# Optimization experiments

Measured on AMD Instinct MI355X. Metric: run time of the kernel, lower is better.

Reference implementation:

```python
import jax, jax.numpy as jnp
import numpy as np

D_MODEL = 1024
NUM_HEADS = 16
D_K = D_MODEL // NUM_HEADS


def setup_inputs() -> dict:
    key = jax.random.key(0)
    ks = jax.random.split(key, 5)
    scale = 1.0 / np.sqrt(D_MODEL)
    x = jax.random.normal(ks[0], (4, 2048, D_MODEL), dtype=jnp.float32)
    W_qkv = jax.random.normal(ks[1], (D_MODEL, 3 * D_MODEL), dtype=jnp.float32) * scale
    b_qkv = jax.random.normal(ks[2], (3 * D_MODEL,), dtype=jnp.float32) * 0.02
    W_o = jax.random.normal(ks[3], (D_MODEL, D_MODEL), dtype=jnp.float32) * scale
    b_o = jax.random.normal(ks[4], (D_MODEL,), dtype=jnp.float32) * 0.02
    return {"x": x, "W_qkv": W_qkv, "b_qkv": b_qkv, "W_o": W_o, "b_o": b_o}


def reference(x, W_qkv, b_qkv, W_o, b_o):
    B, S, _ = x.shape
    qkv = x @ W_qkv + b_qkv  # [B, S, 3*D]
    q, k, v = jnp.split(qkv, 3, axis=-1)
    # [B, H, S, d_k]
    q = q.reshape(B, S, NUM_HEADS, D_K).transpose(0, 2, 1, 3)
    k = k.reshape(B, S, NUM_HEADS, D_K).transpose(0, 2, 1, 3)
    v = v.reshape(B, S, NUM_HEADS, D_K).transpose(0, 2, 1, 3)
    scores = jnp.einsum("bhqd,bhkd->bhqk", q, k) / jnp.sqrt(jnp.float32(D_K))
    causal = jnp.tril(jnp.ones((S, S), dtype=bool))  # [S, S]
    scores = jnp.where(causal[None, None], scores, jnp.float32(-1e9))
    attn = jax.nn.softmax(scores, axis=-1)
    out = jnp.einsum("bhqk,bhkd->bhqd", attn, v)  # [B, H, S, d_k]
    out = out.transpose(0, 2, 1, 3).reshape(B, S, D_MODEL)
    return out @ W_o + b_o
```

## Files before the change

kernel.cpp:

```cpp
#include <hip/hip_runtime.h>
#include <cstdint>
#include <cstddef>

typedef __bf16 bf16x8 __attribute__((ext_vector_type(8)));
typedef __bf16 bf16x4 __attribute__((ext_vector_type(4)));
typedef short s16x4 __attribute__((ext_vector_type(4)));
typedef float f32x4 __attribute__((ext_vector_type(4)));

__device__ __forceinline__ ushort f2bf(float f) {
  union { float f; uint32_t u; } v; v.f = f;
  uint32_t r = (v.u + 0x7fffu + ((v.u >> 16) & 1u)) >> 16;
  return (ushort)r;
}

__device__ __forceinline__ float fast_exp2(float x) {
#if defined(__HIP_DEVICE_COMPILE__) && __has_builtin(__builtin_amdgcn_exp2f)
  return __builtin_amdgcn_exp2f(x);
#else
  return exp2f(x);
#endif
}

__device__ __forceinline__ f32x4 mfma16(bf16x4 a, bf16x4 b, f32x4 c) {
#if defined(__HIP_DEVICE_COMPILE__)
#if __has_builtin(__builtin_amdgcn_mfma_f32_16x16x16_bf16)
  return __builtin_amdgcn_mfma_f32_16x16x16_bf16(a, b, c, 0, 0, 0);
#else
  return __builtin_amdgcn_mfma_f32_16x16x16bf16_1k(
      __builtin_bit_cast(s16x4, a), __builtin_bit_cast(s16x4, b), c, 0, 0, 0);
#endif
#else
  (void)a; (void)b;
  return c;
#endif
}

__device__ __forceinline__ void glds16(const ushort* g, ushort* l) {
  __builtin_amdgcn_global_load_lds((const __attribute__((address_space(1))) void*)g,
                                   (__attribute__((address_space(3))) void*)l, 16, 0, 0);
}

__global__ void prep_all(const float* __restrict__ x, const float* __restrict__ Wqkv,
                         const float* __restrict__ Wo, ushort* __restrict__ xbf,
                         ushort* __restrict__ Wqkv_t, ushort* __restrict__ Wo_t) {
  __shared__ ushort t[32][33];
  const int bid = blockIdx.x;
  const int tid = threadIdx.x;
  if (bid < 8192) {
    const int i = bid * 256 + tid;
    float4 v = ((const float4*)x)[i];
    ushort4 o;
    o.x = f2bf(v.x); o.y = f2bf(v.y); o.z = f2bf(v.z); o.w = f2bf(v.w);
    ((ushort4*)xbf)[i] = o;
    return;
  }
  const int pb = bid - 8192;
  const int bx = pb & 127;
  const int by = pb >> 7;
  const float* in;
  ushort* out;
  int C, c0;
  if (bx < 96) { in = Wqkv; out = Wqkv_t; C = 3072; c0 = bx * 32; }
  else         { in = Wo;   out = Wo_t;   C = 1024; c0 = (bx - 96) * 32; }
  const int R = 1024;
  const int r0 = by * 32;
  const int tx = tid & 31, ty = tid >> 5;
#pragma unroll
  for (int i = 0; i < 4; ++i)
    t[ty + i * 8][tx] = f2bf(in[(size_t)(r0 + ty + i * 8) * C + c0 + tx]);
  __syncthreads();
#pragma unroll
  for (int i = 0; i < 4; ++i)
    out[(size_t)(c0 + ty + i * 8) * R + r0 + tx] = t[tx][ty + i * 8];
}

#define BAR8() do { asm volatile("" ::: "memory"); \
                    __builtin_amdgcn_s_barrier();  \
                    asm volatile("" ::: "memory"); } while (0)
#define VMC4()  asm volatile("s_waitcnt vmcnt(4)" ::: "memory")
#define VMC0()  asm volatile("s_waitcnt vmcnt(0)" ::: "memory")
#define LGKM0() asm volatile("s_waitcnt lgkmcnt(0)" ::: "memory")

template <int MODE>
__launch_bounds__(256, 3)
__global__ void gemm_tb(const ushort* __restrict__ A, const ushort* __restrict__ Bt,
                        const float* __restrict__ bias,
                        ushort* __restrict__ o0, ushort* __restrict__ o1,
                        ushort* __restrict__ o2, float* __restrict__ of,
                        int M, int N, int K) {
  __shared__ ushort smem[24576];
  const int NT = K >> 5;
  const int tid = threadIdx.x;
  const int wid = tid >> 6;
  const int lane = tid & 63;
  const int quad = lane >> 4;
  const int l16 = lane & 15;
  const int wm = (wid >> 1) * 64;
  const int wn = (wid & 1) * 64;

  int wg = blockIdx.y * gridDim.x + blockIdx.x;
  const int ntx = gridDim.x;
  const int cpx = (ntx * gridDim.y) >> 3;
  wg = (wg & 7) * cpx + (wg >> 3);
  const int m0 = (wg / ntx) * 128;
  const int n0 = (wg % ntx) * 128;

  const int r_l = lane >> 2;
  const int q_l = ((lane & 3) - (r_l >> 1)) & 3;
  const ushort* gA0 = A + (size_t)(m0 + wid * 32 + r_l) * K + q_l * 8;
  const ushort* gB0 = Bt + (size_t)(n0 + wid * 32 + r_l) * K + q_l * 8;
  ushort* dA0 = smem + wid * 1024 + lane * 8;
  ushort* dB0 = smem + 12288 + wid * 1024 + lane * 8;

  auto stage = [&](int t, int bs) {
    const ushort* sa = gA0 + t * 32;
    ushort* da = dA0 + bs * 4096;
    glds16(sa, da);
    glds16(sa + 16 * K, da + 512);
    const ushort* sb = gB0 + t * 32;
    ushort* db = dB0 + bs * 4096;
    glds16(sb, db);
    glds16(sb + 16 * K, db + 512);
  };

  const int slot8 = (l16 * 4 + ((quad + (l16 >> 1)) & 3)) * 8;
  const int abase = (wm >> 4) * 512 + slot8;
  const int bbase = 12288 + (wn >> 4) * 512 + slot8;

  f32x4 acc[4][4];
#pragma unroll
  for (int i = 0; i < 4; ++i)
#pragma unroll
    for (int j = 0; j < 4; ++j) acc[i][j] = (f32x4){0.f, 0.f, 0.f, 0.f};

  stage(0, 0);
  stage(1, 1);
  VMC4();
  BAR8();

  int b = 0;
  for (int t = 0; t < NT; ++t) {
    bf16x8 af[4], bfr[4];
    const int boff = b * 4096;
#pragma unroll
    for (int i = 0; i < 4; ++i)
      af[i] = *(const bf16x8*)(smem + boff + abase + i * 512);
#pragma unroll
    for (int j = 0; j < 4; ++j)
      bfr[j] = *(const bf16x8*)(smem + boff + bbase + j * 512);
    const int b2 = (b == 0) ? 2 : b - 1;
    if (t + 2 < NT) stage(t + 2, b2);
    __builtin_amdgcn_s_setprio(1);
#pragma unroll
    for (int i = 0; i < 4; ++i)
#pragma unroll
      for (int j = 0; j < 4; ++j)
        acc[i][j] = __builtin_amdgcn_mfma_f32_16x16x32_bf16(af[i], bfr[j], acc[i][j], 0, 0, 0);
    __builtin_amdgcn_s_setprio(0);
    if (t + 2 < NT) { VMC4(); } else if (t + 1 < NT) { VMC0(); }
    LGKM0();
    BAR8();
    b = (b == 2) ? 0 : b + 1;
  }

  if (MODE == 1) {
#pragma unroll
    for (int i = 0; i < 4; ++i)
#pragma unroll
      for (int j = 0; j < 4; ++j) {
        const int col = n0 + wn + j * 16 + l16;
        const float bv = bias[col];
#pragma unroll
        for (int r = 0; r < 4; ++r) {
          const int row = m0 + wm + i * 16 + quad * 4 + r;
          of[(size_t)row * N + col] = acc[i][j][r] + bv;
        }
      }
  } else {
    const int bb = m0 >> 11;
    const int s0 = m0 & 2047;
    const int wr = wid >> 1;
    const int wcol = wid & 1;
#pragma unroll
    for (int hc = 0; hc < 2; ++hc) {
      const int gc0 = n0 + hc * 64;
      const int sel = gc0 >> 10;
      const int head = (gc0 & 1023) >> 6;
      const size_t bh = (size_t)(bb * 16 + head);
      __syncthreads();
      if (wcol == hc) {
#pragma unroll
        for (int j = 0; j < 4; ++j) {
          const int dloc = j * 16 + l16;
          const float bv = bias[gc0 + dloc];
#pragma unroll
          for (int i = 0; i < 4; ++i) {
#pragma unroll
            for (int r = 0; r < 4; ++r) {
              const int R = wr * 64 + i * 16 + quad * 4 + r;
              float v = acc[i][j][r] + bv;
              if (sel == 0) v *= 0.18033688011112042f;
              const ushort u = f2bf(v);
              if (sel == 2) {
                const int lc = R >> 3;
                smem[dloc * 128 + ((lc ^ (dloc & 7)) << 3) + (R & 7)] = u;
              } else {
                smem[R * 64 + (((dloc >> 3) ^ (R & 7)) << 3) + (dloc & 7)] = u;
              }
            }
          }
        }
      }
      __syncthreads();
      if (sel != 2) {
        ushort* o = sel ? o1 : o0;
        const int R = tid >> 1;
        const int gh = tid & 1;
        ushort* dst = o + (bh * 2048 + s0 + R) * 64 + gh * 32;
        const int key = R & 7;
        const uint4* srow = (const uint4*)(smem + R * 64);
#pragma unroll
        for (int g = 0; g < 4; ++g)
          ((uint4*)dst)[g] = srow[(gh * 4 + g) ^ key];
      } else {
        const int d = tid >> 2;
        const int sq = tid & 3;
        ushort* dst = o2 + (((size_t)(bh * 32 + (s0 >> 6) + (sq >> 1))) << 12) +
                      d * 64 + (sq & 1) * 32;
        const uint4* srow = (const uint4*)(smem + d * 128);
#pragma unroll
        for (int g = 0; g < 4; ++g)
          ((uint4*)dst)[g] = srow[(sq * 4 + g) ^ (d & 7)];
      }
    }
  }
}

__launch_bounds__(256)
__global__ void attn_fused(const ushort* __restrict__ Qb, const ushort* __restrict__ Kb,
                           const ushort* __restrict__ Vt, ushort* __restrict__ Ob) {
  int wg0 = blockIdx.y * 8 + blockIdx.x;
  const int w = (wg0 & 7) * 64 + (wg0 >> 3);
  const int bh = w >> 3;
  const int pair = w & 7;
  const int tid = threadIdx.x;
  const int wid = tid >> 6;
  const int lane = tid & 63;
  const int quad = lane >> 4;
  const int l16 = lane & 15;

  __shared__ ushort Ks[3][2][64 * 32];
  __shared__ ushort Vs[3][2][64 * 32];

  const int lr = lane >> 2;
  const int jphys = lane & 3;
  const int skey = (lr >> 1) & 3;
  const int jlog = jphys ^ skey;
  const int srow = wid * 16 + lr;
  const ushort* KgL = Kb + (size_t)bh * 2048 * 64 + (size_t)srow * 64 + jlog * 8;
  const ushort* VgL = Vt + (size_t)bh * 32 * 4096 + (size_t)srow * 64 + jlog * 8;
  ushort* ldsK0[3], *ldsK1[3], *ldsV0[3], *ldsV1[3];
#pragma unroll
  for (int buf = 0; buf < 3; ++buf) {
    ldsK0[buf] = &Ks[buf][0][wid * 16 * 32] + lane * 8;
    ldsK1[buf] = &Ks[buf][1][wid * 16 * 32] + lane * 8;
    ldsV0[buf] = &Vs[buf][0][wid * 16 * 32] + lane * 8;
    ldsV1[buf] = &Vs[buf][1][wid * 16 * 32] + lane * 8;
  }
  auto stage = [&](int jt, int buf) {
    const ushort* ks = KgL + (size_t)jt * 4096;
    const ushort* vs = VgL + (size_t)jt * 4096;
    glds16(ks, ldsK0[buf]);
    glds16(ks + 32, ldsK1[buf]);
    glds16(vs, ldsV0[buf]);
    glds16(vs + 32, ldsV1[buf]);
  };

  const int rkey = (l16 >> 1) & 3;
  const int b = bh >> 4, h = bh & 15;

  auto process = [&](int qt) {
    const int qg0 = qt * 128 + wid * 32;

    const ushort* Qg = Qb + ((size_t)bh * 2048 + qg0) * 64;
    bf16x8 qa[2][2];
#pragma unroll
    for (int f = 0; f < 2; ++f)
#pragma unroll
      for (int hh = 0; hh < 2; ++hh)
        qa[f][hh] = *(const bf16x8*)(Qg + (f * 16 + l16) * 64 + hh * 32 + quad * 8);

    f32x4 o[2][4];
    float rs[2];
#pragma unroll
    for (int f = 0; f < 2; ++f) {
      rs[f] = 0.f;
#pragma unroll
      for (int m = 0; m < 4; ++m) o[f][m] = (f32x4){0.f, 0.f, 0.f, 0.f};
    }

    const int nIt = 2 * qt + 2;
    stage(0, 0);
    stage(1, 1);

    int buf = 0;
    for (int jt = 0; jt < nIt; ++jt) {
      if (jt + 1 < nIt) { VMC4(); } else { VMC0(); }
      LGKM0();
      BAR8();
      const int b2 = (buf == 0) ? 2 : buf - 1;
      if (jt + 2 < nIt) stage(jt + 2, b2);

      const int kvb = jt * 64;
      if (kvb <= qg0 + 31) {
        f32x4 s[2][4];
        __builtin_amdgcn_s_setprio(1);
#pragma unroll
        for (int n = 0; n < 4; ++n) {
          const int koff = (n * 16 + l16) * 32 + (quad ^ rkey) * 8;
          bf16x8 kb0 = *(const bf16x8*)&Ks[buf][0][koff];
          bf16x8 kb1 = *(const bf16x8*)&Ks[buf][1][koff];
#pragma unroll
          for (int f = 0; f < 2; ++f) {
            f32x4 z = (f32x4){0.f, 0.f, 0.f, 0.f};
            z = __builtin_amdgcn_mfma_f32_16x16x32_bf16(kb0, qa[f][0], z, 0, 0, 0);
            z = __builtin_amdgcn_mfma_f32_16x16x32_bf16(kb1, qa[f][1], z, 0, 0, 0);
            s[f][n] = z;
          }
        }
        __builtin_amdgcn_s_setprio(0);

        bf16x4 p[2][4];
        if (kvb + 63 <= qg0) {
#pragma unroll
          for (int f = 0; f < 2; ++f)
#pragma unroll
            for (int n = 0; n < 4; ++n) {
              float pe[4];
#pragma unroll
              for (int r = 0; r < 4; ++r) {
                pe[r] = fast_exp2(s[f][n][r]);
                rs[f] += pe[r];
              }
              p[f][n] = (bf16x4){(__bf16)pe[0], (__bf16)pe[1], (__bf16)pe[2], (__bf16)pe[3]};
            }
        } else {
#pragma unroll
          for (int f = 0; f < 2; ++f) {
            const int qg = qg0 + f * 16 + l16;
#pragma unroll
            for (int n = 0; n < 4; ++n) {
              const int kg0 = kvb + n * 16 + quad * 4;
              float pe[4];
#pragma unroll
              for (int r = 0; r < 4; ++r) {
                float e = fast_exp2(s[f][n][r]);
                pe[r] = (kg0 + r > qg) ? 0.f : e;
                rs[f] += pe[r];
              }
              p[f][n] = (bf16x4){(__bf16)pe[0], (__bf16)pe[1], (__bf16)pe[2], (__bf16)pe[3]};
            }
          }
        }

        __builtin_amdgcn_s_setprio(1);
#pragma unroll
        for (int m = 0; m < 4; ++m) {
          const int vrow = (m * 16 + l16) * 32;
#pragma unroll
          for (int n = 0; n < 4; ++n) {
            const int clog = (n & 1) * 2 + (quad >> 1);
            const int voff = vrow + (clog ^ rkey) * 8 + (quad & 1) * 4;
            bf16x4 va = *(const bf16x4*)&Vs[buf][n >> 1][voff];
#pragma unroll
            for (int f = 0; f < 2; ++f) o[f][m] = mfma16(va, p[f][n], o[f][m]);
          }
        }
        __builtin_amdgcn_s_setprio(0);
      }
      buf = (buf == 2) ? 0 : buf + 1;
    }

#pragma unroll
    for (int f = 0; f < 2; ++f) {
      float t = rs[f];
      t += __shfl_xor(t, 16, 64);
      t += __shfl_xor(t, 32, 64);
      const float il = 1.f / t;
      const int q = qg0 + f * 16 + l16;
      ushort* dst = Ob + ((size_t)b * 2048 + q) * 1024 + h * 64;
#pragma unroll
      for (int m = 0; m < 4; ++m) {
        ushort4 w2;
        w2.x = f2bf(o[f][m][0] * il);
        w2.y = f2bf(o[f][m][1] * il);
        w2.z = f2bf(o[f][m][2] * il);
        w2.w = f2bf(o[f][m][3] * il);
        *(ushort4*)(dst + m * 16 + quad * 4) = w2;
      }
    }
  };

  process(15 - pair);
  __syncthreads();
  process(pair);
}

extern "C" void kernel_launch(void* const* d_in, const int* in_sizes, int n_in,
                              void* d_out, int out_size, void* d_ws, size_t ws_size,
                              hipStream_t stream) {
  const float* x    = (const float*)d_in[0];
  const float* Wqkv = (const float*)d_in[1];
  const float* bqkv = (const float*)d_in[2];
  const float* Wo   = (const float*)d_in[3];
  const float* bo   = (const float*)d_in[4];
  float* out = (float*)d_out;

  char* ws = (char*)d_ws;
  size_t off = 0;
  auto alloc = [&](size_t bytes) {
    void* p = ws + off;
    off += (bytes + 255) & ~(size_t)255;
    return p;
  };
  ushort* xbf    = (ushort*)alloc((size_t)8192 * 1024 * 2);
  ushort* Wqkv_t = (ushort*)alloc((size_t)3072 * 1024 * 2);
  ushort* Wo_t   = (ushort*)alloc((size_t)1024 * 1024 * 2);
  ushort* Qb     = (ushort*)alloc((size_t)64 * 2048 * 64 * 2);
  ushort* Kb     = (ushort*)alloc((size_t)64 * 2048 * 64 * 2);
  ushort* Vb     = (ushort*)alloc((size_t)64 * 2048 * 64 * 2);
  ushort* Ab     = (ushort*)alloc((size_t)8192 * 1024 * 2);

  prep_all<<<dim3(12288), dim3(256), 0, stream>>>(x, Wqkv, Wo, xbf, Wqkv_t, Wo_t);
  gemm_tb<0><<<dim3(24, 64), dim3(256), 0, stream>>>(xbf, Wqkv_t, bqkv, Qb, Kb, Vb, nullptr,
                                                     8192, 3072, 1024);
  attn_fused<<<dim3(8, 64), dim3(256), 0, stream>>>(Qb, Kb, Vb, Ab);
  gemm_tb<1><<<dim3(8, 64), dim3(256), 0, stream>>>(Ab, Wo_t, bo, nullptr, nullptr, nullptr,
                                                    out, 8192, 1024, 1024);
}
```

Baseline: 269.4 us.

## Share K/V tile loads between paired high and low query tiles in one pass

Rather than processing the high query tile and then the low query tile in two separate passes, each with its own K/V streaming, the kernel now runs a single loop over the high tile's key range. Each staged K/V tile feeds both query tiles while the low tile is still inside its causal range. This removes the second pass's redundant global-to-LDS traffic and barriers. It doubles the live accumulator and Q registers, and adds a launch-bounds occupancy hint of 2 to keep register pressure in check, with a risk of spills or lower occupancy.

```diff
diff --git a/kernel.cpp b/kernel.cpp
--- a/kernel.cpp
+++ b/kernel.cpp
@@ -236,7 +236,7 @@
   }
 }
 
-__launch_bounds__(256)
+__launch_bounds__(256, 2)
 __global__ void attn_fused(const ushort* __restrict__ Qb, const ushort* __restrict__ Kb,
                            const ushort* __restrict__ Vt, ushort* __restrict__ Ob) {
   int wg0 = blockIdx.y * 8 + blockIdx.x;
@@ -279,108 +279,123 @@
   const int rkey = (l16 >> 1) & 3;
   const int b = bh >> 4, h = bh & 15;
 
-  auto process = [&](int qt) {
-    const int qg0 = qt * 128 + wid * 32;
-
-    const ushort* Qg = Qb + ((size_t)bh * 2048 + qg0) * 64;
-    bf16x8 qa[2][2];
+  const int qtH = 15 - pair;
+  const int qtL = pair;
+  const int qg0H = qtH * 128 + wid * 32;
+  const int qg0L = qtL * 128 + wid * 32;
+  const int nHi = 2 * qtH + 2;
+
+  bf16x8 qaH[2][2], qaL[2][2];
+  {
+    const ushort* QgH = Qb + ((size_t)bh * 2048 + qg0H) * 64;
+    const ushort* QgL = Qb + ((size_t)bh * 2048 + qg0L) * 64;
 #pragma unroll
     for (int f = 0; f < 2; ++f)
 #pragma unroll
-      for (int hh = 0; hh < 2; ++hh)
-        qa[f][hh] = *(const bf16x8*)(Qg + (f * 16 + l16) * 64 + hh * 32 + quad * 8);
-
-    f32x4 o[2][4];
-    float rs[2];
-#pragma unroll
-    for (int f = 0; f < 2; ++f) {
-      rs[f] = 0.f;
-#pragma unroll
-      for (int m = 0; m < 4; ++m) o[f][m] = (f32x4){0.f, 0.f, 0.f, 0.f};
-    }
-
-    const int nIt = 2 * qt + 2;
-    stage(0, 0);
-    stage(1, 1);
-
-    int buf = 0;
-    for (int jt = 0; jt < nIt; ++jt) {
-      if (jt + 1 < nIt) { VMC4(); } else { VMC0(); }
-      LGKM0();
-      BAR8();
-      const int b2 = (buf == 0) ? 2 : buf - 1;
-      if (jt + 2 < nIt) stage(jt + 2, b2);
-
-      const int kvb = jt * 64;
-      if (kvb <= qg0 + 31) {
-        f32x4 s[2][4];
-        __builtin_amdgcn_s_setprio(1);
+      for (int hh = 0; hh < 2; ++hh) {
+        qaH[f][hh] = *(const bf16x8*)(QgH + (f * 16 + l16) * 64 + hh * 32 + quad * 8);
+        qaL[f][hh] = *(const bf16x8*)(QgL + (f * 16 + l16) * 64 + hh * 32 + quad * 8);
+      }
+  }
+
+  f32x4 oH[2][4], oL[2][4];
+  float rsH[2], rsL[2];
+#pragma unroll
+  for (int f = 0; f < 2; ++f) {
+    rsH[f] = 0.f; rsL[f] = 0.f;
+#pragma unroll
+    for (int m = 0; m < 4; ++m) {
+      oH[f][m] = (f32x4){0.f, 0.f, 0.f, 0.f};
+      oL[f][m] = (f32x4){0.f, 0.f, 0.f, 0.f};
+    }
+  }
+
+  auto computeTile = [&](bf16x8 (&qa)[2][2], f32x4 (&o)[2][4], float (&rs)[2],
+                         int qg0, int kvb, int buf) {
+    f32x4 s[2][4];
+    __builtin_amdgcn_s_setprio(1);
+#pragma unroll
+    for (int n = 0; n < 4; ++n) {
+      const int koff = (n * 16 + l16) * 32 + (quad ^ rkey) * 8;
+      bf16x8 kb0 = *(const bf16x8*)&Ks[buf][0][koff];
+      bf16x8 kb1 = *(const bf16x8*)&Ks[buf][1][koff];
+#pragma unroll
+      for (int f = 0; f < 2; ++f) {
+        f32x4 z = (f32x4){0.f, 0.f, 0.f, 0.f};
+        z = __builtin_amdgcn_mfma_f32_16x16x32_bf16(kb0, qa[f][0], z, 0, 0, 0);
+        z = __builtin_amdgcn_mfma_f32_16x16x32_bf16(kb1, qa[f][1], z, 0, 0, 0);
+        s[f][n] = z;
+      }
+    }
+    __builtin_amdgcn_s_setprio(0);
+
+    bf16x4 p[2][4];
+    if (kvb + 63 <= qg0) {
+#pragma unroll
+      for (int f = 0; f < 2; ++f)
 #pragma unroll
         for (int n = 0; n < 4; ++n) {
-          const int koff = (n * 16 + l16) * 32 + (quad ^ rkey) * 8;
-          bf16x8 kb0 = *(const bf16x8*)&Ks[buf][0][koff];
-          bf16x8 kb1 = *(const bf16x8*)&Ks[buf][1][koff];
-#pragma unroll
-          for (int f = 0; f < 2; ++f) {
-            f32x4 z = (f32x4){0.f, 0.f, 0.f, 0.f};
-            z = __builtin_amdgcn_mfma_f32_16x16x32_bf16(kb0, qa[f][0], z, 0, 0, 0);
-            z = __builtin_amdgcn_mfma_f32_16x16x32_bf16(kb1, qa[f][1], z, 0, 0, 0);
-            s[f][n] = z;
+          float pe[4];
+#pragma unroll
+          for (int r = 0; r < 4; ++r) {
+            pe[r] = fast_exp2(s[f][n][r]);
+            rs[f] += pe[r];
           }
+          p[f][n] = (bf16x4){(__bf16)pe[0], (__bf16)pe[1], (__bf16)pe[2], (__bf16)pe[3]};
         }
-        __builtin_amdgcn_s_setprio(0);
-
-        bf16x4 p[2][4];
-        if (kvb + 63 <= qg0) {
-#pragma unroll
-          for (int f = 0; f < 2; ++f)
-#pragma unroll
-            for (int n = 0; n < 4; ++n) {
-              float pe[4];
-#pragma unroll
-              for (int r = 0; r < 4; ++r) {
-                pe[r] = fast_exp2(s[f][n][r]);
-                rs[f] += pe[r];
-              }
-              p[f][n] = (bf16x4){(__bf16)pe[0], (__bf16)pe[1], (__bf16)pe[2], (__bf16)pe[3]};
-            }
-        } else {
-#pragma unroll
-          for (int f = 0; f < 2; ++f) {
-            const int qg = qg0 + f * 16 + l16;
-#pragma unroll
-            for (int n = 0; n < 4; ++n) {
-              const int kg0 = kvb + n * 16 + quad * 4;
-              float pe[4];
-#pragma unroll
-              for (int r = 0; r < 4; ++r) {
-                float e = fast_exp2(s[f][n][r]);
-                pe[r] = (kg0 + r > qg) ? 0.f : e;
-                rs[f] += pe[r];
-              }
-              p[f][n] = (bf16x4){(__bf16)pe[0], (__bf16)pe[1], (__bf16)pe[2], (__bf16)pe[3]};
-            }
+    } else {
+#pragma unroll
+      for (int f = 0; f < 2; ++f) {
+        const int qg = qg0 + f * 16 + l16;
+#pragma unroll
+        for (int n = 0; n < 4; ++n) {
+          const int kg0 = kvb + n * 16 + quad * 4;
+          float pe[4];
+#pragma unroll
+          for (int r = 0; r < 4; ++r) {
+            float e = fast_exp2(s[f][n][r]);
+            pe[r] = (kg0 + r > qg) ? 0.f : e;
+            rs[f] += pe[r];
           }
+          p[f][n] = (bf16x4){(__bf16)pe[0], (__bf16)pe[1], (__bf16)pe[2], (__bf16)pe[3]};
         }
-
-        __builtin_amdgcn_s_setprio(1);
-#pragma unroll
-        for (int m = 0; m < 4; ++m) {
-          const int vrow = (m * 16 + l16) * 32;
-#pragma unroll
-          for (int n = 0; n < 4; ++n) {
-            const int clog = (n & 1) * 2 + (quad >> 1);
-            const int voff = vrow + (clog ^ rkey) * 8 + (quad & 1) * 4;
-            bf16x4 va = *(const bf16x4*)&Vs[buf][n >> 1][voff];
-#pragma unroll
-            for (int f = 0; f < 2; ++f) o[f][m] = mfma16(va, p[f][n], o[f][m]);
-          }
-        }
-        __builtin_amdgcn_s_setprio(0);
-      }
-      buf = (buf == 2) ? 0 : buf + 1;
-    }
-
+      }
+    }
+
+    __builtin_amdgcn_s_setprio(1);
+#pragma unroll
+    for (int m = 0; m < 4; ++m) {
+      const int vrow = (m * 16 + l16) * 32;
+#pragma unroll
+      for (int n = 0; n < 4; ++n) {
+        const int clog = (n & 1) * 2 + (quad >> 1);
+        const int voff = vrow + (clog ^ rkey) * 8 + (quad & 1) * 4;
+        bf16x4 va = *(const bf16x4*)&Vs[buf][n >> 1][voff];
+#pragma unroll
+        for (int f = 0; f < 2; ++f) o[f][m] = mfma16(va, p[f][n], o[f][m]);
+      }
+    }
+    __builtin_amdgcn_s_setprio(0);
+  };
+
+  stage(0, 0);
+  stage(1, 1);
+
+  int buf = 0;
+  for (int jt = 0; jt < nHi; ++jt) {
+    if (jt + 1 < nHi) { VMC4(); } else { VMC0(); }
+    LGKM0();
+    BAR8();
+    const int b2 = (buf == 0) ? 2 : buf - 1;
+    if (jt + 2 < nHi) stage(jt + 2, b2);
+
+    const int kvb = jt * 64;
+    if (kvb <= qg0H + 31) computeTile(qaH, oH, rsH, qg0H, kvb, buf);
+    if (kvb <= qg0L + 31) computeTile(qaL, oL, rsL, qg0L, kvb, buf);
+    buf = (buf == 2) ? 0 : buf + 1;
+  }
+
+  auto writeO = [&](f32x4 (&o)[2][4], float (&rs)[2], int qg0) {
 #pragma unroll
     for (int f = 0; f < 2; ++f) {
       float t = rs[f];
@@ -400,10 +415,8 @@
       }
     }
   };
-
-  process(15 - pair);
-  __syncthreads();
-  process(pair);
+  writeO(oH, rsH, qg0H);
+  writeO(oL, rsL, qg0L);
 }
 
 extern "C" void kernel_launch(void* const* d_in, const int* in_sizes, int n_in,
```

Result: faster. 254.7 us (-5.5%).
